# Kernel tuning notes

Measured on AMD Instinct MI355X. Metric: run time of the kernel, lower is better.

## Reference

```python
import jax, jax.numpy as jnp
from jax import lax
import numpy as np

EPS = 1e-5
RADIUS = 0.2
NPOINT = 1024
NSAMPLE = 32
B, N = 8, 8192


def furthest_point_sample(xyz, npoint):
    # xyz: (B,N,3) -> idx (B,npoint), start at index 0 (pytorch3d default)
    Bn, Nn, _ = xyz.shape
    def step(carry, _):
        dists, last = carry  # (B,N), (B,)
        lastpt = jnp.take_along_axis(xyz, last[:, None, None], axis=1)  # (B,1,3)
        d = jnp.sum((xyz - lastpt) ** 2, axis=-1)  # (B,N)
        dists = jnp.minimum(dists, d)
        nxt = jnp.argmax(dists, axis=-1).astype(jnp.int32)
        return (dists, nxt), last
    init = (jnp.full((Bn, Nn), jnp.inf, xyz.dtype), jnp.zeros((Bn,), jnp.int32))
    _, idxs = lax.scan(step, init, None, length=npoint)  # (npoint,B)
    return idxs.T  # (B,npoint)


def ball_query(radius, nsample, xyz, new_xyz):
    # first `nsample` points (by original index order) within radius; pad -> 0 (clamp of -1)
    Nn = xyz.shape[1]
    d2 = jnp.sum((new_xyz[:, :, None, :] - xyz[:, None, :, :]) ** 2, axis=-1)  # (B,S,N)
    valid = d2 < radius * radius
    score = jnp.where(valid, jnp.arange(Nn, dtype=jnp.int32), jnp.int32(Nn))  # smaller = earlier valid
    neg_vals, _ = lax.top_k(-score, nsample)  # picks nsample smallest scores
    idx = -neg_vals  # (B,S,nsample)
    idx = jnp.where(idx == Nn, 0, idx)  # pytorch3d pads with -1, then clamp(min=0) -> 0
    return idx


def bn_relu(x, g, be, m, v):
    # eval-mode BatchNorm over channel (last) dim + ReLU
    return jax.nn.relu((x - m) * (g / jnp.sqrt(v + EPS)) + be)


def setup_inputs() -> dict:
    key = jax.random.key(0)
    ks = jax.random.split(key, 4)
    xyz = jax.random.uniform(ks[0], (B, N, 3), dtype=jnp.float32)
    w1 = jax.random.normal(ks[1], (64, 3), dtype=jnp.float32) * 0.1
    w2 = jax.random.normal(ks[2], (64, 64), dtype=jnp.float32) * 0.1
    w3 = jax.random.normal(ks[3], (128, 64), dtype=jnp.float32) * 0.1
    z64, o64 = jnp.zeros((64,), jnp.float32), jnp.ones((64,), jnp.float32)
    z128, o128 = jnp.zeros((128,), jnp.float32), jnp.ones((128,), jnp.float32)
    return {
        "xyz": xyz,
        "w1": w1, "b1": z64, "g1": o64, "be1": z64, "m1": z64, "v1": o64,
        "w2": w2, "b2": z64, "g2": o64, "be2": z64, "m2": z64, "v2": o64,
        "w3": w3, "b3": z128, "g3": o128, "be3": z128, "m3": z128, "v3": o128,
    }


def reference(xyz, w1, b1, g1, be1, m1, v1, w2, b2, g2, be2, m2, v2, w3, b3, g3, be3, m3, v3):
    fps_idx = furthest_point_sample(xyz, NPOINT)  # (B,npoint)
    new_xyz = jnp.take_along_axis(xyz, fps_idx[:, :, None], axis=1)  # (B,npoint,3)
    idx = ball_query(RADIUS, NSAMPLE, xyz, new_xyz)  # (B,npoint,nsample)
    grouped_xyz = jax.vmap(lambda pts, i: pts[i])(xyz, idx)  # (B,npoint,nsample,3)
    # 1x1 conv MLP (channels-last) + eval BN + ReLU
    h = bn_relu(jnp.einsum('bsnc,oc->bsno', grouped_xyz, w1) + b1, g1, be1, m1, v1)
    h = bn_relu(jnp.einsum('bsnc,oc->bsno', h, w2) + b2, g2, be2, m2, v2)
    h = bn_relu(jnp.einsum('bsnc,oc->bsno', h, w3) + b3, g3, be3, m3, v3)
    new_features = jnp.max(h, axis=2)  # (B,npoint,128) max over nsample
    new_features = jnp.transpose(new_features, (0, 2, 1))  # (B,128,npoint) to match torch layout
    return new_xyz, new_features
```

## Files before the change

kernel.cpp:

```cpp
#include <hip/hip_runtime.h>

#define B 8
#define N 8192
#define S 1024
#define NS 32
constexpr float BN_EPS = 1e-5f;

typedef float v2f __attribute__((ext_vector_type(2)));

__device__ __forceinline__ float wave_max_to_lane63(float x) {
  int v = __float_as_int(x);
#define DPP_MAX(ctrl)                                                     \
  v = __float_as_int(fmaxf(__int_as_float(v),                             \
      __int_as_float(__builtin_amdgcn_update_dpp(v, v, (ctrl), 0xf, 0xf, \
                                                 false))))
  DPP_MAX(0x111);
  DPP_MAX(0x112);
  DPP_MAX(0x114);
  DPP_MAX(0x118);
  DPP_MAX(0x142);
  DPP_MAX(0x143);
#undef DPP_MAX
  return __int_as_float(v);
}

#define FPS_T 512

__global__ void __attribute__((amdgpu_flat_work_group_size(FPS_T, FPS_T),
                               amdgpu_waves_per_eu(2, 2)))
k_fps(const float* __restrict__ xyz, float* __restrict__ new_xyz) {
#pragma clang fp contract(off)
  extern __shared__ float4 s_xyz4[];
  __shared__ alignas(16) float s_ctr[S * 3];
  __shared__ unsigned long long s_red[2][8];
  const int b = blockIdx.x;
  const int t = threadIdx.x;
  const int lane = t & 63;
  const int w = t >> 6;
  const float* base = xyz + (size_t)b * N * 3;
  v2f X[8], Y[8], Z[8], D[8];
  const int p0 = t * 16;
  {
    const float4* src = (const float4*)(base + (size_t)p0 * 3);
    float buf[48];
#pragma unroll
    for (int i = 0; i < 12; ++i) {
      float4 v = src[i];
      buf[4 * i + 0] = v.x; buf[4 * i + 1] = v.y;
      buf[4 * i + 2] = v.z; buf[4 * i + 3] = v.w;
    }
#pragma unroll
    for (int k = 0; k < 16; ++k) {
      s_xyz4[p0 + k] =
          make_float4(buf[3 * k], buf[3 * k + 1], buf[3 * k + 2], 0.f);
    }
#pragma unroll
    for (int i = 0; i < 8; ++i) {
      X[i] = (v2f){buf[6 * i + 0], buf[6 * i + 3]};
      Y[i] = (v2f){buf[6 * i + 1], buf[6 * i + 4]};
      Z[i] = (v2f){buf[6 * i + 2], buf[6 * i + 5]};
      D[i] = (v2f){3.4e38f, 3.4e38f};
    }
  }
  float lx = base[0], ly = base[1], lz = base[2];
  if (t == 0) {
    s_ctr[0] = lx; s_ctr[1] = ly; s_ctr[2] = lz;
  }
  for (int r = 1; r < S; ++r) {
    v2f lx2 = lx, ly2 = ly, lz2 = lz;
#pragma unroll
    for (int i = 0; i < 8; ++i) {
      v2f dx = X[i] - lx2, dy = Y[i] - ly2, dz = Z[i] - lz2;
      v2f d = (dx * dx + dy * dy) + dz * dz;
      D[i] = __builtin_elementwise_min(D[i], d);
    }
    float n1[8], n2[4], n3[2];
#pragma unroll
    for (int i = 0; i < 8; ++i) n1[i] = fmaxf(D[i].x, D[i].y);
#pragma unroll
    for (int i = 0; i < 4; ++i) n2[i] = fmaxf(n1[2 * i], n1[2 * i + 1]);
    n3[0] = fmaxf(n2[0], n2[1]);
    n3[1] = fmaxf(n2[2], n2[3]);
    float m = fmaxf(n3[0], n3[1]);
    int c3 = (n3[0] < m) ? 1 : 0;
    float n2s = c3 ? n2[2] : n2[0];
    int c2 = (n2s < m) ? 1 : 0;
    float n1a = c3 ? n1[4] : n1[0];
    float n1b = c3 ? n1[6] : n1[2];
    float n1s = c2 ? n1b : n1a;
    int c1 = (n1s < m) ? 1 : 0;
    float dx0 = c3 ? D[4].x : D[0].x;
    float dx1 = c3 ? D[5].x : D[1].x;
    float dx2 = c3 ? D[6].x : D[2].x;
    float dx3 = c3 ? D[7].x : D[3].x;
    float dxa = c2 ? dx2 : dx0;
    float dxb = c2 ? dx3 : dx1;
    float dxs = c1 ? dxb : dxa;
    int c0 = (dxs < m) ? 1 : 0;
    int li = 8 * c3 + 4 * c2 + 2 * c1 + c0;
    float wm = wave_max_to_lane63(m);
    float wavemax = __int_as_float(
        __builtin_amdgcn_readlane(__float_as_int(wm), 63));
    unsigned long long bal = __ballot(m == wavemax);
    int firstlane = (int)__builtin_ctzll(bal);
    int widx = __builtin_amdgcn_readlane(p0 + li, firstlane);
    unsigned long long key =
        ((unsigned long long)__float_as_uint(wavemax) << 32) |
        (unsigned)(8191 - widx);
    if (lane == 0) s_red[r & 1][w] = key;
    __syncthreads();
    {
      const unsigned long long* sr = s_red[r & 1];
      unsigned long long k0 = sr[0], k1 = sr[1], k2 = sr[2], k3 = sr[3];
      unsigned long long k4 = sr[4], k5 = sr[5], k6 = sr[6], k7 = sr[7];
      unsigned long long a = k0 > k1 ? k0 : k1;
      unsigned long long c = k2 > k3 ? k2 : k3;
      unsigned long long e = k4 > k5 ? k4 : k5;
      unsigned long long g = k6 > k7 ? k6 : k7;
      unsigned long long ac = a > c ? a : c;
      unsigned long long eg = e > g ? e : g;
      unsigned long long kmax = ac > eg ? ac : eg;
      const int bi = 8191 - (int)(unsigned)(kmax & 0xffffffffull);
      float4 cc = s_xyz4[bi];
      lx = cc.x; ly = cc.y; lz = cc.z;
    }
    if (t == 0) {
      s_ctr[r * 3 + 0] = lx; s_ctr[r * 3 + 1] = ly; s_ctr[r * 3 + 2] = lz;
    }
  }
  __syncthreads();
  float* o = new_xyz + (size_t)b * S * 3;
  for (int i = t; i < (S * 3) / 4; i += FPS_T) {
    ((float4*)o)[i] = ((const float4*)s_ctr)[i];
  }
}

__global__ __launch_bounds__(256) void k_ball(const float* __restrict__ xyz,
                                              const float* __restrict__ new_xyz,
                                              int* __restrict__ ball_idx) {
#pragma clang fp contract(off)
  constexpr float R2 = (float)(0.2 * 0.2);
  const int t = threadIdx.x;
  const int wv = (blockIdx.x << 2) + (t >> 6);
  const int lane = t & 63;
  const int b = wv >> 10;
  const float* base = xyz + (size_t)b * N * 3;
  const float* c = new_xyz + (size_t)wv * 3;
  float cx = c[0], cy = c[1], cz = c[2];
  int* out = ball_idx + (size_t)wv * NS;
  int cnt = 0;
  for (int c0 = 0; c0 < N && cnt < NS; c0 += 64) {
    int p = c0 + lane;
    float x = base[p * 3], y = base[p * 3 + 1], z = base[p * 3 + 2];
    float dx = x - cx, dy = y - cy, dz = z - cz;
    float d = (dx * dx + dy * dy) + dz * dz;
    bool v = d < R2;
    unsigned long long mk = __ballot(v);
    int rank = cnt + __popcll(mk & ((1ull << lane) - 1ull));
    if (v && rank < NS) out[rank] = p;
    cnt += (int)__popcll(mk);
  }
  if (cnt < NS)
    for (int j = cnt + lane; j < NS; j += 64) out[j] = 0;
}

__global__ void __attribute__((amdgpu_flat_work_group_size(256, 256),
                               amdgpu_waves_per_eu(2, 2)))
k_mlp(const float* __restrict__ xyz, const int* __restrict__ ball_idx,
      const float* __restrict__ w1, const float* __restrict__ b1,
      const float* __restrict__ g1, const float* __restrict__ be1,
      const float* __restrict__ m1, const float* __restrict__ v1,
      const float* __restrict__ w2, const float* __restrict__ b2,
      const float* __restrict__ g2, const float* __restrict__ be2,
      const float* __restrict__ m2, const float* __restrict__ v2,
      const float* __restrict__ w3, const float* __restrict__ b3,
      const float* __restrict__ g3, const float* __restrict__ be3,
      const float* __restrict__ m3, const float* __restrict__ v3,
      float* __restrict__ out_feat) {
  const int t = threadIdx.x;
  const int w = t >> 6, lane = t & 63;
  const int wv = (blockIdx.x << 2) + w;
  const int b = wv >> 10, s = wv & (S - 1);
  __shared__ float sh[4][NS * 64];
  __shared__ float sc[4][NS * 4];
  float* h = sh[w];
  float* cs = sc[w];
  const int* gi = ball_idx + (size_t)wv * NS;
  const float* base = xyz + (size_t)b * N * 3;
  if (lane < NS) {
    int p = gi[lane];
    cs[lane * 4 + 0] = base[p * 3 + 0];
    cs[lane * 4 + 1] = base[p * 3 + 1];
    cs[lane * 4 + 2] = base[p * 3 + 2];
  }
  __syncthreads();
  {
    float sv = g1[lane] / sqrtf(v1[lane] + BN_EPS);
    float bb = (b1[lane] - m1[lane]) * sv + be1[lane];
    float wx = w1[lane * 3 + 0] * sv, wy = w1[lane * 3 + 1] * sv,
          wz = w1[lane * 3 + 2] * sv;
    for (int n = 0; n < NS; ++n) {
      float a = fmaf(wx, cs[n * 4 + 0],
                     fmaf(wy, cs[n * 4 + 1], fmaf(wz, cs[n * 4 + 2], bb)));
      h[n * 64 + lane] = fmaxf(a, 0.f);
    }
  }
  __syncthreads();
  {
    float sv = g2[lane] / sqrtf(v2[lane] + BN_EPS);
    float bb = (b2[lane] - m2[lane]) * sv + be2[lane];
    float W[64];
#pragma unroll
    for (int k = 0; k < 64; k += 4) {
      float4 q = *(const float4*)(w2 + lane * 64 + k);
      W[k + 0] = q.x * sv; W[k + 1] = q.y * sv;
      W[k + 2] = q.z * sv; W[k + 3] = q.w * sv;
    }
    for (int n = 0; n < NS; ++n) {
      float acc = bb;
#pragma unroll
      for (int k = 0; k < 64; k += 4) {
        float4 q = *(const float4*)(h + n * 64 + k);
        acc = fmaf(W[k + 0], q.x, acc);
        acc = fmaf(W[k + 1], q.y, acc);
        acc = fmaf(W[k + 2], q.z, acc);
        acc = fmaf(W[k + 3], q.w, acc);
      }
      h[n * 64 + lane] = fmaxf(acc, 0.f);
    }
  }
  __syncthreads();
  float mxa = 0.f, mxb = 0.f;
  {
    float sva = g3[lane] / sqrtf(v3[lane] + BN_EPS);
    float bba = (b3[lane] - m3[lane]) * sva + be3[lane];
    float svb = g3[lane + 64] / sqrtf(v3[lane + 64] + BN_EPS);
    float bbb = (b3[lane + 64] - m3[lane + 64]) * svb + be3[lane + 64];
    float Wa[64], Wb[64];
#pragma unroll
    for (int k = 0; k < 64; k += 4) {
      float4 qa = *(const float4*)(w3 + lane * 64 + k);
      Wa[k + 0] = qa.x * sva; Wa[k + 1] = qa.y * sva;
      Wa[k + 2] = qa.z * sva; Wa[k + 3] = qa.w * sva;
      float4 qb = *(const float4*)(w3 + (lane + 64) * 64 + k);
      Wb[k + 0] = qb.x * svb; Wb[k + 1] = qb.y * svb;
      Wb[k + 2] = qb.z * svb; Wb[k + 3] = qb.w * svb;
    }
    for (int n = 0; n < NS; ++n) {
      float acca = bba, accb = bbb;
#pragma unroll
      for (int k = 0; k < 64; k += 4) {
        float4 q = *(const float4*)(h + n * 64 + k);
        acca = fmaf(Wa[k + 0], q.x, acca);
        acca = fmaf(Wa[k + 1], q.y, acca);
        acca = fmaf(Wa[k + 2], q.z, acca);
        acca = fmaf(Wa[k + 3], q.w, acca);
        accb = fmaf(Wb[k + 0], q.x, accb);
        accb = fmaf(Wb[k + 1], q.y, accb);
        accb = fmaf(Wb[k + 2], q.z, accb);
        accb = fmaf(Wb[k + 3], q.w, accb);
      }
      mxa = fmaxf(mxa, acca);
      mxb = fmaxf(mxb, accb);
    }
  }
  out_feat[((size_t)b * 128 + lane) * S + s] = mxa;
  out_feat[((size_t)b * 128 + 64 + lane) * S + s] = mxb;
}

extern "C" void kernel_launch(void* const* d_in, const int* in_sizes, int n_in,
                              void* d_out, int out_size, void* d_ws,
                              size_t ws_size, hipStream_t stream) {
  const float* xyz = (const float*)d_in[0];
  const float* w1 = (const float*)d_in[1];
  const float* b1 = (const float*)d_in[2];
  const float* g1 = (const float*)d_in[3];
  const float* be1 = (const float*)d_in[4];
  const float* m1 = (const float*)d_in[5];
  const float* v1 = (const float*)d_in[6];
  const float* w2 = (const float*)d_in[7];
  const float* b2 = (const float*)d_in[8];
  const float* g2 = (const float*)d_in[9];
  const float* be2 = (const float*)d_in[10];
  const float* m2 = (const float*)d_in[11];
  const float* v2 = (const float*)d_in[12];
  const float* w3 = (const float*)d_in[13];
  const float* b3 = (const float*)d_in[14];
  const float* g3 = (const float*)d_in[15];
  const float* be3 = (const float*)d_in[16];
  const float* m3 = (const float*)d_in[17];
  const float* v3 = (const float*)d_in[18];

  float* out = (float*)d_out;
  float* new_xyz = out;
  float* out_feat = out + (size_t)B * S * 3;
  int* ball = (int*)d_ws;

  k_fps<<<B, FPS_T, N * sizeof(float4), stream>>>(xyz, new_xyz);
  k_ball<<<(B * S) / 4, 256, 0, stream>>>(xyz, new_xyz, ball);
  k_mlp<<<(B * S) / 4, 256, 0, stream>>>(xyz, ball, w1, b1, g1, be1, m1, v1,
                                         w2, b2, g2, be2, m2, v2, w3, b3, g3,
                                         be3, m3, v3, out_feat);
}
```

Measured before the change: 1.066 ms.

## Fuse FPS, ball query and MLP into one producer-consumer persistent kernel

Merges the three kernels into a single cooperative launch. Eight blocks run furthest point sampling and publish centers to global memory in groups of eight, raising a per-batch progress counter with a release store. The remaining blocks act as persistent consumers that spin on those counters, then run ball query and the MLP for each center as soon as it is available. The ball-query result now goes straight into shared memory instead of a workspace round trip. The aim is to overlap the long serial FPS phase with the grouping and MLP work and to drop two launches, at the cost of spin-wait polling, a hard requirement that all blocks be co-resident, and the loss of occupancy the old MLP kernel had.

```diff
diff --git a/kernel.cpp b/kernel.cpp
--- a/kernel.cpp
+++ b/kernel.cpp
@@ -4,9 +4,23 @@
 #define N 8192
 #define S 1024
 #define NS 32
+#define THREADS 512
+#define NCONS_BLK 248
+#define NCONS_WAVE (NCONS_BLK * 8)
 constexpr float BN_EPS = 1e-5f;
 
 typedef float v2f __attribute__((ext_vector_type(2)));
+
+struct KParams {
+  const float* xyz;
+  const float *w1, *b1, *g1, *be1, *m1, *v1;
+  const float *w2, *b2, *g2, *be2, *m2, *v2;
+  const float *w3, *b3, *g3, *be3, *m3, *v3;
+  float* new_xyz;
+  float* out_feat;
+  float* ctrs;
+  unsigned* prog;
+};
 
 __device__ __forceinline__ float wave_max_to_lane63(float x) {
   int v = __float_as_int(x);
@@ -24,20 +38,14 @@
   return __int_as_float(v);
 }
 
-#define FPS_T 512
-
-__global__ void __attribute__((amdgpu_flat_work_group_size(FPS_T, FPS_T),
-                               amdgpu_waves_per_eu(2, 2)))
-k_fps(const float* __restrict__ xyz, float* __restrict__ new_xyz) {
+__device__ __forceinline__ void producer(const KParams& P, char* smem, int b,
+                                         int t, int lane, int w) {
 #pragma clang fp contract(off)
-  extern __shared__ float4 s_xyz4[];
-  __shared__ alignas(16) float s_ctr[S * 3];
-  __shared__ unsigned long long s_red[2][8];
-  const int b = blockIdx.x;
-  const int t = threadIdx.x;
-  const int lane = t & 63;
-  const int w = t >> 6;
-  const float* base = xyz + (size_t)b * N * 3;
+  float4* s_xyz4 = (float4*)smem;
+  float* s_ctr = (float*)(smem + 131072);
+  unsigned long long(*s_red)[8] =
+      (unsigned long long(*)[8])(smem + 131072 + 12288);
+  const float* base = P.xyz + (size_t)b * N * 3;
   v2f X[8], Y[8], Z[8], D[8];
   const int p0 = t * 16;
   {
@@ -50,10 +58,9 @@
       buf[4 * i + 2] = v.z; buf[4 * i + 3] = v.w;
     }
 #pragma unroll
-    for (int k = 0; k < 16; ++k) {
+    for (int k = 0; k < 16; ++k)
       s_xyz4[p0 + k] =
           make_float4(buf[3 * k], buf[3 * k + 1], buf[3 * k + 2], 0.f);
-    }
 #pragma unroll
     for (int i = 0; i < 8; ++i) {
       X[i] = (v2f){buf[6 * i + 0], buf[6 * i + 3]};
@@ -63,9 +70,7 @@
     }
   }
   float lx = base[0], ly = base[1], lz = base[2];
-  if (t == 0) {
-    s_ctr[0] = lx; s_ctr[1] = ly; s_ctr[2] = lz;
-  }
+  if (t == 0) { s_ctr[0] = lx; s_ctr[1] = ly; s_ctr[2] = lz; }
   for (int r = 1; r < S; ++r) {
     v2f lx2 = lx, ly2 = ly, lz2 = lz;
 #pragma unroll
@@ -99,8 +104,8 @@
     int c0 = (dxs < m) ? 1 : 0;
     int li = 8 * c3 + 4 * c2 + 2 * c1 + c0;
     float wm = wave_max_to_lane63(m);
-    float wavemax = __int_as_float(
-        __builtin_amdgcn_readlane(__float_as_int(wm), 63));
+    float wavemax =
+        __int_as_float(__builtin_amdgcn_readlane(__float_as_int(wm), 63));
     unsigned long long bal = __ballot(m == wavemax);
     int firstlane = (int)__builtin_ctzll(bal);
     int widx = __builtin_amdgcn_readlane(p0 + li, firstlane);
@@ -127,125 +132,112 @@
     if (t == 0) {
       s_ctr[r * 3 + 0] = lx; s_ctr[r * 3 + 1] = ly; s_ctr[r * 3 + 2] = lz;
     }
+    if (w == 0 && (r & 7) == 7) {
+      int cbase = (r - 7) * 3;
+      if (lane < 24) {
+        float v = s_ctr[cbase + lane];
+        __hip_atomic_store(P.ctrs + (size_t)b * (S * 3) + cbase + lane, v,
+                           __ATOMIC_RELAXED, __HIP_MEMORY_SCOPE_AGENT);
+      }
+      if (lane == 0)
+        __hip_atomic_store(&P.prog[b * 64], (unsigned)(r + 1),
+                           __ATOMIC_RELEASE, __HIP_MEMORY_SCOPE_AGENT);
+    }
   }
   __syncthreads();
-  float* o = new_xyz + (size_t)b * S * 3;
-  for (int i = t; i < (S * 3) / 4; i += FPS_T) {
+  float* o = P.new_xyz + (size_t)b * S * 3;
+  for (int i = t; i < (S * 3) / 4; i += THREADS)
     ((float4*)o)[i] = ((const float4*)s_ctr)[i];
-  }
-}
-
-__global__ __launch_bounds__(256) void k_ball(const float* __restrict__ xyz,
-                                              const float* __restrict__ new_xyz,
-                                              int* __restrict__ ball_idx) {
+}
+
+__device__ __forceinline__ void consumer(const KParams& P, char* smem, int cid,
+                                         int t, int lane, int w) {
 #pragma clang fp contract(off)
   constexpr float R2 = (float)(0.2 * 0.2);
-  const int t = threadIdx.x;
-  const int wv = (blockIdx.x << 2) + (t >> 6);
-  const int lane = t & 63;
-  const int b = wv >> 10;
-  const float* base = xyz + (size_t)b * N * 3;
-  const float* c = new_xyz + (size_t)wv * 3;
-  float cx = c[0], cy = c[1], cz = c[2];
-  int* out = ball_idx + (size_t)wv * NS;
-  int cnt = 0;
-  for (int c0 = 0; c0 < N && cnt < NS; c0 += 64) {
-    int p = c0 + lane;
-    float x = base[p * 3], y = base[p * 3 + 1], z = base[p * 3 + 2];
-    float dx = x - cx, dy = y - cy, dz = z - cz;
-    float d = (dx * dx + dy * dy) + dz * dz;
-    bool v = d < R2;
-    unsigned long long mk = __ballot(v);
-    int rank = cnt + __popcll(mk & ((1ull << lane) - 1ull));
-    if (v && rank < NS) out[rank] = p;
-    cnt += (int)__popcll(mk);
-  }
-  if (cnt < NS)
-    for (int j = cnt + lane; j < NS; j += 64) out[j] = 0;
-}
-
-__global__ void __attribute__((amdgpu_flat_work_group_size(256, 256),
-                               amdgpu_waves_per_eu(2, 2)))
-k_mlp(const float* __restrict__ xyz, const int* __restrict__ ball_idx,
-      const float* __restrict__ w1, const float* __restrict__ b1,
-      const float* __restrict__ g1, const float* __restrict__ be1,
-      const float* __restrict__ m1, const float* __restrict__ v1,
-      const float* __restrict__ w2, const float* __restrict__ b2,
-      const float* __restrict__ g2, const float* __restrict__ be2,
-      const float* __restrict__ m2, const float* __restrict__ v2,
-      const float* __restrict__ w3, const float* __restrict__ b3,
-      const float* __restrict__ g3, const float* __restrict__ be3,
-      const float* __restrict__ m3, const float* __restrict__ v3,
-      float* __restrict__ out_feat) {
-  const int t = threadIdx.x;
-  const int w = t >> 6, lane = t & 63;
-  const int wv = (blockIdx.x << 2) + w;
-  const int b = wv >> 10, s = wv & (S - 1);
-  __shared__ float sh[4][NS * 64];
-  __shared__ float sc[4][NS * 4];
-  float* h = sh[w];
-  float* cs = sc[w];
-  const int* gi = ball_idx + (size_t)wv * NS;
-  const float* base = xyz + (size_t)b * N * 3;
-  if (lane < NS) {
-    int p = gi[lane];
-    cs[lane * 4 + 0] = base[p * 3 + 0];
-    cs[lane * 4 + 1] = base[p * 3 + 1];
-    cs[lane * 4 + 2] = base[p * 3 + 2];
-  }
-  __syncthreads();
-  {
-    float sv = g1[lane] / sqrtf(v1[lane] + BN_EPS);
-    float bb = (b1[lane] - m1[lane]) * sv + be1[lane];
-    float wx = w1[lane * 3 + 0] * sv, wy = w1[lane * 3 + 1] * sv,
-          wz = w1[lane * 3 + 2] * sv;
+  float* h = (float*)smem + w * (NS * 64);
+  float* cs = (float*)smem + 8 * NS * 64 + w * (NS * 4);
+  const unsigned gw = cid * 8 + w;
+  float sv1 = P.g1[lane] / sqrtf(P.v1[lane] + BN_EPS);
+  float bb1 = (P.b1[lane] - P.m1[lane]) * sv1 + P.be1[lane];
+  float w1x = P.w1[lane * 3 + 0] * sv1, w1y = P.w1[lane * 3 + 1] * sv1,
+        w1z = P.w1[lane * 3 + 2] * sv1;
+  float sv2 = P.g2[lane] / sqrtf(P.v2[lane] + BN_EPS);
+  float bb2 = (P.b2[lane] - P.m2[lane]) * sv2 + P.be2[lane];
+  float W2[64];
+#pragma unroll
+  for (int k = 0; k < 64; k += 4) {
+    float4 q = *(const float4*)(P.w2 + lane * 64 + k);
+    W2[k + 0] = q.x * sv2; W2[k + 1] = q.y * sv2;
+    W2[k + 2] = q.z * sv2; W2[k + 3] = q.w * sv2;
+  }
+  float sva = P.g3[lane] / sqrtf(P.v3[lane] + BN_EPS);
+  float bba = (P.b3[lane] - P.m3[lane]) * sva + P.be3[lane];
+  float svb = P.g3[lane + 64] / sqrtf(P.v3[lane + 64] + BN_EPS);
+  float bbb = (P.b3[lane + 64] - P.m3[lane + 64]) * svb + P.be3[lane + 64];
+  float Wa[64], Wb[64];
+#pragma unroll
+  for (int k = 0; k < 64; k += 4) {
+    float4 qa = *(const float4*)(P.w3 + lane * 64 + k);
+    Wa[k + 0] = qa.x * sva; Wa[k + 1] = qa.y * sva;
+    Wa[k + 2] = qa.z * sva; Wa[k + 3] = qa.w * sva;
+    float4 qb = *(const float4*)(P.w3 + (lane + 64) * 64 + k);
+    Wb[k + 0] = qb.x * svb; Wb[k + 1] = qb.y * svb;
+    Wb[k + 2] = qb.z * svb; Wb[k + 3] = qb.w * svb;
+  }
+  for (unsigned c = gw; c < B * S; c += NCONS_WAVE) {
+    const int b = c & 7;
+    const int s = c >> 3;
+    while (__hip_atomic_load(&P.prog[b * 64], __ATOMIC_RELAXED,
+                             __HIP_MEMORY_SCOPE_AGENT) <= (unsigned)s)
+      __builtin_amdgcn_s_sleep(2);
+    (void)__hip_atomic_load(&P.prog[b * 64], __ATOMIC_ACQUIRE,
+                            __HIP_MEMORY_SCOPE_AGENT);
+    const float* cg = P.ctrs + (size_t)b * (S * 3) + s * 3;
+    float cx = __hip_atomic_load(cg + 0, __ATOMIC_RELAXED,
+                                 __HIP_MEMORY_SCOPE_AGENT);
+    float cy = __hip_atomic_load(cg + 1, __ATOMIC_RELAXED,
+                                 __HIP_MEMORY_SCOPE_AGENT);
+    float cz = __hip_atomic_load(cg + 2, __ATOMIC_RELAXED,
+                                 __HIP_MEMORY_SCOPE_AGENT);
+    const float* base = P.xyz + (size_t)b * N * 3;
+    int cnt = 0;
+    for (int c0 = 0; c0 < N && cnt < NS; c0 += 64) {
+      int p = c0 + lane;
+      float x = base[p * 3], y = base[p * 3 + 1], z = base[p * 3 + 2];
+      float dx = x - cx, dy = y - cy, dz = z - cz;
+      float d = (dx * dx + dy * dy) + dz * dz;
+      bool v = d < R2;
+      unsigned long long mk = __ballot(v);
+      int rank = cnt + __popcll(mk & ((1ull << lane) - 1ull));
+      if (v && rank < NS) {
+        cs[rank * 4 + 0] = x; cs[rank * 4 + 1] = y; cs[rank * 4 + 2] = z;
+      }
+      cnt += (int)__popcll(mk);
+    }
+    if (cnt < NS) {
+      float x0 = base[0], y0 = base[1], z0 = base[2];
+      for (int j = cnt + lane; j < NS; j += 64) {
+        cs[j * 4 + 0] = x0; cs[j * 4 + 1] = y0; cs[j * 4 + 2] = z0;
+      }
+    }
     for (int n = 0; n < NS; ++n) {
-      float a = fmaf(wx, cs[n * 4 + 0],
-                     fmaf(wy, cs[n * 4 + 1], fmaf(wz, cs[n * 4 + 2], bb)));
+      float a = fmaf(w1x, cs[n * 4 + 0],
+                     fmaf(w1y, cs[n * 4 + 1], fmaf(w1z, cs[n * 4 + 2], bb1)));
       h[n * 64 + lane] = fmaxf(a, 0.f);
     }
-  }
-  __syncthreads();
-  {
-    float sv = g2[lane] / sqrtf(v2[lane] + BN_EPS);
-    float bb = (b2[lane] - m2[lane]) * sv + be2[lane];
-    float W[64];
-#pragma unroll
-    for (int k = 0; k < 64; k += 4) {
-      float4 q = *(const float4*)(w2 + lane * 64 + k);
-      W[k + 0] = q.x * sv; W[k + 1] = q.y * sv;
-      W[k + 2] = q.z * sv; W[k + 3] = q.w * sv;
-    }
     for (int n = 0; n < NS; ++n) {
-      float acc = bb;
+      float acc = bb2;
 #pragma unroll
       for (int k = 0; k < 64; k += 4) {
         float4 q = *(const float4*)(h + n * 64 + k);
-        acc = fmaf(W[k + 0], q.x, acc);
-        acc = fmaf(W[k + 1], q.y, acc);
-        acc = fmaf(W[k + 2], q.z, acc);
-        acc = fmaf(W[k + 3], q.w, acc);
+        acc = fmaf(W2[k + 0], q.x, acc);
+        acc = fmaf(W2[k + 1], q.y, acc);
+        acc = fmaf(W2[k + 2], q.z, acc);
+        acc = fmaf(W2[k + 3], q.w, acc);
       }
       h[n * 64 + lane] = fmaxf(acc, 0.f);
     }
-  }
-  __syncthreads();
-  float mxa = 0.f, mxb = 0.f;
-  {
-    float sva = g3[lane] / sqrtf(v3[lane] + BN_EPS);
-    float bba = (b3[lane] - m3[lane]) * sva + be3[lane];
-    float svb = g3[lane + 64] / sqrtf(v3[lane + 64] + BN_EPS);
-    float bbb = (b3[lane + 64] - m3[lane + 64]) * svb + be3[lane + 64];
-    float Wa[64], Wb[64];
-#pragma unroll
-    for (int k = 0; k < 64; k += 4) {
-      float4 qa = *(const float4*)(w3 + lane * 64 + k);
-      Wa[k + 0] = qa.x * sva; Wa[k + 1] = qa.y * sva;
-      Wa[k + 2] = qa.z * sva; Wa[k + 3] = qa.w * sva;
-      float4 qb = *(const float4*)(w3 + (lane + 64) * 64 + k);
-      Wb[k + 0] = qb.x * svb; Wb[k + 1] = qb.y * svb;
-      Wb[k + 2] = qb.z * svb; Wb[k + 3] = qb.w * svb;
-    }
+    float mxa = 0.f, mxb = 0.f;
     for (int n = 0; n < NS; ++n) {
       float acca = bba, accb = bbb;
 #pragma unroll
@@ -263,42 +255,52 @@
       mxa = fmaxf(mxa, acca);
       mxb = fmaxf(mxb, accb);
     }
-  }
-  out_feat[((size_t)b * 128 + lane) * S + s] = mxa;
-  out_feat[((size_t)b * 128 + 64 + lane) * S + s] = mxb;
+    P.out_feat[((size_t)b * 128 + lane) * S + s] = mxa;
+    P.out_feat[((size_t)b * 128 + 64 + lane) * S + s] = mxb;
+  }
+}
+
+__global__ void __attribute__((amdgpu_flat_work_group_size(THREADS, THREADS),
+                               amdgpu_waves_per_eu(2, 2)))
+k_fused(KParams P) {
+  extern __shared__ char smem[];
+  const int t = threadIdx.x;
+  const int lane = t & 63;
+  const int w = t >> 6;
+  if (blockIdx.x < B)
+    producer(P, smem, blockIdx.x, t, lane, w);
+  else
+    consumer(P, smem, blockIdx.x - B, t, lane, w);
 }
 
 extern "C" void kernel_launch(void* const* d_in, const int* in_sizes, int n_in,
                               void* d_out, int out_size, void* d_ws,
                               size_t ws_size, hipStream_t stream) {
-  const float* xyz = (const float*)d_in[0];
-  const float* w1 = (const float*)d_in[1];
-  const float* b1 = (const float*)d_in[2];
-  const float* g1 = (const float*)d_in[3];
-  const float* be1 = (const float*)d_in[4];
-  const float* m1 = (const float*)d_in[5];
-  const float* v1 = (const float*)d_in[6];
-  const float* w2 = (const float*)d_in[7];
-  const float* b2 = (const float*)d_in[8];
-  const float* g2 = (const float*)d_in[9];
-  const float* be2 = (const float*)d_in[10];
-  const float* m2 = (const float*)d_in[11];
-  const float* v2 = (const float*)d_in[12];
-  const float* w3 = (const float*)d_in[13];
-  const float* b3 = (const float*)d_in[14];
-  const float* g3 = (const float*)d_in[15];
-  const float* be3 = (const float*)d_in[16];
-  const float* m3 = (const float*)d_in[17];
-  const float* v3 = (const float*)d_in[18];
-
+  KParams P;
+  P.xyz = (const float*)d_in[0];
+  P.w1 = (const float*)d_in[1];  P.b1 = (const float*)d_in[2];
+  P.g1 = (const float*)d_in[3];  P.be1 = (const float*)d_in[4];
+  P.m1 = (const float*)d_in[5];  P.v1 = (const float*)d_in[6];
+  P.w2 = (const float*)d_in[7];  P.b2 = (const float*)d_in[8];
+  P.g2 = (const float*)d_in[9];  P.be2 = (const float*)d_in[10];
+  P.m2 = (const float*)d_in[11]; P.v2 = (const float*)d_in[12];
+  P.w3 = (const float*)d_in[13]; P.b3 = (const float*)d_in[14];
+  P.g3 = (const float*)d_in[15]; P.be3 = (const float*)d_in[16];
+  P.m3 = (const float*)d_in[17]; P.v3 = (const float*)d_in[18];
   float* out = (float*)d_out;
-  float* new_xyz = out;
-  float* out_feat = out + (size_t)B * S * 3;
-  int* ball = (int*)d_ws;
-
-  k_fps<<<B, FPS_T, N * sizeof(float4), stream>>>(xyz, new_xyz);
-  k_ball<<<(B * S) / 4, 256, 0, stream>>>(xyz, new_xyz, ball);
-  k_mlp<<<(B * S) / 4, 256, 0, stream>>>(xyz, ball, w1, b1, g1, be1, m1, v1,
-                                         w2, b2, g2, be2, m2, v2, w3, b3, g3,
-                                         be3, m3, v3, out_feat);
-}
+  P.new_xyz = out;
+  P.out_feat = out + (size_t)B * S * 3;
+  P.prog = (unsigned*)d_ws;
+  P.ctrs = (float*)((char*)d_ws + 2048);
+
+  hipMemsetAsync(d_ws, 0, 2048, stream);
+
+  void* args[] = {&P};
+  dim3 grid(B + NCONS_BLK), blk(THREADS);
+  size_t shmem = 131072 + 12288 + 256;
+  hipError_t e = hipLaunchCooperativeKernel((const void*)k_fused, grid, blk,
+                                            args, (unsigned)shmem, stream);
+  if (e != hipSuccess) {
+    k_fused<<<grid, blk, shmem, stream>>>(P);
+  }
+}
```

After: 1.049 ms. Within noise of the previous version (-1.6%).
